# Kernel tuning notes

Measured on AMD Instinct MI355X. Metric: run time of the kernel, lower is better.

## Reference

```python
import jax, jax.numpy as jnp
import numpy as np

TEMP = 0.05


def _l2norm(x, axis=-1, eps=1e-12):
    n = jnp.sqrt(jnp.sum(x * x, axis=axis, keepdims=True))
    return x / jnp.maximum(n, eps)


def setup_inputs() -> dict:
    key = jax.random.key(0)
    k1, k2, k3 = jax.random.split(key, 3)
    B, D, N = 1024, 2048, 16384
    inputs = jax.random.normal(k1, (B, D), dtype=jnp.float32)
    targets = jax.random.randint(k2, (B,), 0, N, dtype=jnp.int32).astype(jnp.int64)
    # cluster memory bank: initialized to unit-norm centroids (buffer is zeros in
    # torch but is always filled with normalized centroids before use)
    features = _l2norm(jax.random.normal(k3, (N, D), dtype=jnp.float32))
    return {"inputs": inputs, "targets": targets, "features": features}


def reference(inputs, targets, features):
    # ClusterMemory.forward: normalize -> cosine sim vs bank -> / temp
    xn = _l2norm(inputs, axis=1)            # [B, D]
    out = (xn @ features.T) / TEMP          # [B, N]
    return out
```

## Files before the change

### kernel.cpp

```cpp
#include <hip/hip_runtime.h>
#include <hip/hip_bf16.h>


typedef short  bf16x8 __attribute__((ext_vector_type(8)));
typedef float  f32x4  __attribute__((ext_vector_type(4)));
typedef float  f32x16 __attribute__((ext_vector_type(16)));

#define D_K   2048
#define N_N   16384
#define M_M   1024
#define TEMP_INV 20.0f

__device__ __forceinline__ unsigned short f2bf(float f) {
    unsigned u = __builtin_bit_cast(unsigned, f);
    u += 0x7FFFu + ((u >> 16) & 1u);
    return (unsigned short)(u >> 16);
}

#define GLOAD16(g, l) __builtin_amdgcn_global_load_lds(                        \
    (const __attribute__((address_space(1))) unsigned int*)(g),                \
    (__attribute__((address_space(3))) unsigned int*)(l), 16, 0, 0)

__global__ __launch_bounds__(256) void prep_kernel(const float* __restrict__ x,
                                                   const float* __restrict__ B,
                                                   unsigned short* __restrict__ abf,
                                                   unsigned short* __restrict__ bbf) {
    int t = threadIdx.x;
    if (blockIdx.x < M_M) {
        int row = blockIdx.x;
        const float4* xr = reinterpret_cast<const float4*>(x + (size_t)row * D_K);
        float4 a = xr[t * 2];
        float4 b = xr[t * 2 + 1];
        float s = a.x*a.x + a.y*a.y + a.z*a.z + a.w*a.w
                + b.x*b.x + b.y*b.y + b.z*b.z + b.w*b.w;
        #pragma unroll
        for (int off = 32; off > 0; off >>= 1) s += __shfl_down(s, off);
        __shared__ float ps[4];
        __shared__ float sbc;
        if ((t & 63) == 0) ps[t >> 6] = s;
        __syncthreads();
        if (t == 0) {
            float tot = ps[0] + ps[1] + ps[2] + ps[3];
            sbc = 1.0f / fmaxf(sqrtf(tot), 1e-12f);
        }
        __syncthreads();
        float rs = sbc;
        bf16x8 v;
        v[0] = (short)f2bf(a.x * rs); v[1] = (short)f2bf(a.y * rs);
        v[2] = (short)f2bf(a.z * rs); v[3] = (short)f2bf(a.w * rs);
        v[4] = (short)f2bf(b.x * rs); v[5] = (short)f2bf(b.y * rs);
        v[6] = (short)f2bf(b.z * rs); v[7] = (short)f2bf(b.w * rs);
        *reinterpret_cast<bf16x8*>(abf + (size_t)row * D_K + t * 8) = v;
    } else {
        const size_t nv = (size_t)N_N * D_K / 8;
        size_t stride = (size_t)(gridDim.x - M_M) * blockDim.x;
        for (size_t v = (size_t)(blockIdx.x - M_M) * blockDim.x + t; v < nv; v += stride) {
            const float4* p = reinterpret_cast<const float4*>(B) + v * 2;
            float4 a = p[0], b = p[1];
            bf16x8 o;
            o[0] = (short)f2bf(a.x); o[1] = (short)f2bf(a.y);
            o[2] = (short)f2bf(a.z); o[3] = (short)f2bf(a.w);
            o[4] = (short)f2bf(b.x); o[5] = (short)f2bf(b.y);
            o[6] = (short)f2bf(b.z); o[7] = (short)f2bf(b.w);
            reinterpret_cast<bf16x8*>(bbf)[v] = o;
        }
    }
}

__global__ __launch_bounds__(512, 2) void gemm32_kernel(const unsigned short* __restrict__ Abf,
                                                        const unsigned short* __restrict__ Bbf,
                                                        float* __restrict__ C) {
    __shared__ __align__(16) unsigned short lds[65536];

    int bid = blockIdx.x;
    int wg  = (bid & 7) * 32 + (bid >> 3);
    int tm  = wg & 3, tn = wg >> 2;
    int m_blk = tm * 256, n_blk = tn * 256;

    int t = threadIdx.x, lane = t & 63, w = t >> 6;
    int wm = w >> 2, wn = w & 3;

    int row31 = lane & 31, khalf = lane >> 5;
    int xorm  = (row31 >> 1) & 3;
    int slotk[2], aao[4], bbo[2];
    #pragma unroll
    for (int kk = 0; kk < 2; ++kk) slotk[kk] = ((kk * 2 + khalf) ^ xorm) * 16;
    #pragma unroll
    for (int rb = 0; rb < 4; ++rb) aao[rb] = (wm * 128 + rb * 32 + row31) * 64;
    #pragma unroll
    for (int cb = 0; cb < 2; ++cb) bbo[cb] = (wn * 64 + cb * 32 + row31) * 64;

    const unsigned short* gA[2];
    const unsigned short* gB[2];
    int sdst[2];
    #pragma unroll
    for (int pass = 0; pass < 2; ++pass) {
        int r = pass * 128 + (t >> 2);
        int csrc = (t & 3) ^ ((r >> 1) & 3);
        gA[pass] = Abf + (size_t)(m_blk + r) * D_K + csrc * 8;
        gB[pass] = Bbf + (size_t)(n_blk + r) * D_K + csrc * 8;
        sdst[pass] = pass * 8192 + w * 1024;
    }

    auto stage = [&](int mat, int s, int b, int ktile) {
        int kt = ktile < 32 ? ktile : 31;
        int koff = kt * 64 + s * 32;
        int ldsb = b * 65536 + mat * 32768 + s * 16384;
        GLOAD16((mat ? gB[0] : gA[0]) + koff, (char*)lds + ldsb + sdst[0]);
        GLOAD16((mat ? gB[1] : gA[1]) + koff, (char*)lds + ldsb + sdst[1]);
    };

    f32x16 acc[4][2] = {};

#define PHASE32(bb, ss, ST1, ST2)                                              \
    {                                                                          \
        char* abase = (char*)lds + (bb) * 65536 + (ss) * 16384;                \
        char* bbase = abase + 32768;                                           \
        bf16x8 af[4][2], bv[2][2];                                             \
        _Pragma("unroll")                                                      \
        for (int rb = 0; rb < 4; ++rb)                                         \
            _Pragma("unroll")                                                  \
            for (int kk = 0; kk < 2; ++kk)                                     \
                af[rb][kk] = *reinterpret_cast<const bf16x8*>(                 \
                    abase + aao[rb] + slotk[kk]);                              \
        _Pragma("unroll")                                                      \
        for (int cb = 0; cb < 2; ++cb)                                         \
            _Pragma("unroll")                                                  \
            for (int kk = 0; kk < 2; ++kk)                                     \
                bv[cb][kk] = *reinterpret_cast<const bf16x8*>(                 \
                    bbase + bbo[cb] + slotk[kk]);                              \
        ST1;                                                                   \
        ST2;                                                                   \
        asm volatile("s_barrier" ::: "memory");                                \
        asm volatile("s_waitcnt lgkmcnt(0)" ::: "memory");                     \
        __builtin_amdgcn_sched_barrier(0);                                     \
        __builtin_amdgcn_s_setprio(1);                                         \
        _Pragma("unroll")                                                      \
        for (int kk = 0; kk < 2; ++kk)                                         \
            _Pragma("unroll")                                                  \
            for (int rb = 0; rb < 4; ++rb)                                     \
                _Pragma("unroll")                                              \
                for (int cb = 0; cb < 2; ++cb)                                 \
                    acc[rb][cb] = __builtin_amdgcn_mfma_f32_32x32x16_bf16(     \
                        af[rb][kk], bv[cb][kk], acc[rb][cb], 0, 0, 0);         \
        __builtin_amdgcn_s_setprio(0);                                         \
        asm volatile("s_waitcnt vmcnt(8)" ::: "memory");                       \
        asm volatile("s_barrier" ::: "memory");                                \
    }

    stage(0, 0, 0, 0);
    stage(1, 0, 0, 0);
    stage(0, 1, 0, 0);
    stage(1, 1, 0, 0);
    stage(0, 0, 1, 1);
    stage(1, 0, 1, 1);
    asm volatile("s_waitcnt vmcnt(8)" ::: "memory");
    asm volatile("s_barrier" ::: "memory");

    for (int T = 0; T < 32; ++T) {
        int b = T & 1;
        PHASE32(b, 0, stage(0, 1, b ^ 1, T + 1), stage(1, 1, b ^ 1, T + 1))
        PHASE32(b, 1, stage(0, 0, b,     T + 2), stage(1, 0, b,     T + 2))
    }
#undef PHASE32

    #pragma unroll
    for (int rb = 0; rb < 4; ++rb)
        #pragma unroll
        for (int cb = 0; cb < 2; ++cb) {
            int colg = n_blk + wn * 64 + cb * 32 + row31;
            #pragma unroll
            for (int r = 0; r < 16; ++r) {
                int rowg = m_blk + wm * 128 + rb * 32 +
                           (r & 3) + 8 * (r >> 2) + 4 * khalf;
                C[(size_t)rowg * N_N + colg] = acc[rb][cb][r] * TEMP_INV;
            }
        }
}

__global__ __launch_bounds__(256) void rnorm_kernel(const float* __restrict__ x,
                                                    float* __restrict__ rn) {
    int row = blockIdx.x;
    const float4* xr = reinterpret_cast<const float4*>(x + (size_t)row * D_K);
    int t = threadIdx.x;
    float4 a = xr[t];
    float4 b = xr[t + 256];
    float s = a.x*a.x + a.y*a.y + a.z*a.z + a.w*a.w
            + b.x*b.x + b.y*b.y + b.z*b.z + b.w*b.w;
    #pragma unroll
    for (int off = 32; off > 0; off >>= 1) s += __shfl_down(s, off);
    __shared__ float ps[4];
    int wave = t >> 6, lane = t & 63;
    if (lane == 0) ps[wave] = s;
    __syncthreads();
    if (t == 0) {
        float tot = ps[0] + ps[1] + ps[2] + ps[3];
        rn[row] = 1.0f / fmaxf(sqrtf(tot), 1e-12f);
    }
}

__global__ __launch_bounds__(256, 2) void gemm_kernel(const float* __restrict__ A,
                                                      const float* __restrict__ Bm,
                                                      const float* __restrict__ rn,
                                                      float* __restrict__ C) {
    constexpr int BK = 64;
    __shared__ __align__(16) short lAs[128 * BK];
    __shared__ __align__(16) short lBs[128 * BK];
    int bid = blockIdx.x;
    int nb  = (bid & 7) * 128 + (bid >> 3);
    int tm  = nb & 7;
    int tn  = nb >> 3;
    int m0 = tm * 128, n0 = tn * 128;
    int t = threadIdx.x;
    int lane = t & 63, w = t >> 6;
    int wr = (w >> 1) * 64, wc = (w & 1) * 64;
    f32x4 acc[4][4] = {};
    float4 ra[4][2], rb[4][2];
    float  sc[4];
    int    srow[4], sgrp[4];
    #pragma unroll
    for (int i = 0; i < 4; ++i) {
        int li = t + i * 256;
        srow[i] = li >> 3;
        sgrp[i] = li & 7;
        sc[i]   = rn[m0 + srow[i]];
    }
    auto load_tiles = [&](int kt) {
        int k0 = kt * BK;
        #pragma unroll
        for (int i = 0; i < 4; ++i) {
            const float4* pa = reinterpret_cast<const float4*>(
                A + (size_t)(m0 + srow[i]) * D_K + k0 + sgrp[i] * 8);
            ra[i][0] = pa[0]; ra[i][1] = pa[1];
            const float4* pb = reinterpret_cast<const float4*>(
                Bm + (size_t)(n0 + srow[i]) * D_K + k0 + sgrp[i] * 8);
            rb[i][0] = pb[0]; rb[i][1] = pb[1];
        }
    };
    auto write_tiles = [&]() {
        #pragma unroll
        for (int i = 0; i < 4; ++i) {
            int row = srow[i];
            int slotw = sgrp[i] ^ (row & 7);
            float s = sc[i];
            bf16x8 va, vb;
            va[0] = (short)f2bf(ra[i][0].x * s); va[1] = (short)f2bf(ra[i][0].y * s);
            va[2] = (short)f2bf(ra[i][0].z * s); va[3] = (short)f2bf(ra[i][0].w * s);
            va[4] = (short)f2bf(ra[i][1].x * s); va[5] = (short)f2bf(ra[i][1].y * s);
            va[6] = (short)f2bf(ra[i][1].z * s); va[7] = (short)f2bf(ra[i][1].w * s);
            vb[0] = (short)f2bf(rb[i][0].x); vb[1] = (short)f2bf(rb[i][0].y);
            vb[2] = (short)f2bf(rb[i][0].z); vb[3] = (short)f2bf(rb[i][0].w);
            vb[4] = (short)f2bf(rb[i][1].x); vb[5] = (short)f2bf(rb[i][1].y);
            vb[6] = (short)f2bf(rb[i][1].z); vb[7] = (short)f2bf(rb[i][1].w);
            *reinterpret_cast<bf16x8*>(&lAs[row * BK + slotw * 8]) = va;
            *reinterpret_cast<bf16x8*>(&lBs[row * BK + slotw * 8]) = vb;
        }
    };
    auto compute = [&]() {
        #pragma unroll
        for (int ks = 0; ks < 2; ++ks) {
            bf16x8 af[4], bfr[4];
            #pragma unroll
            for (int f = 0; f < 4; ++f) {
                int arow = wr + f * 16 + (lane & 15);
                int aslot = (ks * 4 + (lane >> 4)) ^ (arow & 7);
                af[f] = *reinterpret_cast<const bf16x8*>(&lAs[arow * BK + aslot * 8]);
                int brow = wc + f * 16 + (lane & 15);
                int bslot = (ks * 4 + (lane >> 4)) ^ (brow & 7);
                bfr[f] = *reinterpret_cast<const bf16x8*>(&lBs[brow * BK + bslot * 8]);
            }
            #pragma unroll
            for (int m = 0; m < 4; ++m)
                #pragma unroll
                for (int n = 0; n < 4; ++n)
                    acc[m][n] = __builtin_amdgcn_mfma_f32_16x16x32_bf16(
                        af[m], bfr[n], acc[m][n], 0, 0, 0);
        }
    };
    load_tiles(0);
    write_tiles();
    for (int kt = 1; kt < D_K / BK; ++kt) {
        __syncthreads();
        load_tiles(kt);
        compute();
        __syncthreads();
        write_tiles();
    }
    __syncthreads();
    compute();
    #pragma unroll
    for (int m = 0; m < 4; ++m) {
        int r = m0 + wr + m * 16 + (lane >> 4) * 4;
        #pragma unroll
        for (int j = 0; j < 4; ++j) {
            float* cp = C + (size_t)(r + j) * N_N + n0 + wc + (lane & 15);
            #pragma unroll
            for (int n = 0; n < 4; ++n)
                cp[n * 16] = acc[m][n][j] * TEMP_INV;
        }
    }
}

extern "C" void kernel_launch(void* const* d_in, const int* in_sizes, int n_in,
                              void* d_out, int out_size, void* d_ws, size_t ws_size,
                              hipStream_t stream) {
    const float* inputs   = (const float*)d_in[0];
    const float* features = (const float*)d_in[2];
    float* out = (float*)d_out;

    const size_t needA = (size_t)M_M * D_K * 2;
    const size_t needB = (size_t)N_N * D_K * 2;
    if (ws_size >= needA + needB) {
        unsigned short* Abf = (unsigned short*)d_ws;
        unsigned short* Bbf = Abf + (size_t)M_M * D_K;
        prep_kernel<<<M_M + 2048, 256, 0, stream>>>(inputs, features, Abf, Bbf);
        gemm32_kernel<<<(M_M / 256) * (N_N / 256), 512, 0, stream>>>(Abf, Bbf, out);
    } else {
        float* rn = (float*)d_ws;
        rnorm_kernel<<<M_M, 256, 0, stream>>>(inputs, rn);
        gemm_kernel<<<(M_M / 128) * (N_N / 128), 256, 0, stream>>>(inputs, features, rn, out);
    }
}
```

Measured before the change: 113.2 us.

## Switch GEMM to 128x512 tiles with 16x16x32 MFMA and single-block occupancy

Replaces the 256x256-tile GEMM, which used 32x32x16 MFMAs and two blocks per CU, with a 128x512 tile that uses 16x16x32 MFMAs, one block per CU and 160 KB of double-buffered LDS. Each wave now computes a 64x128 sub-tile, and every global-to-LDS stage loads one A slice plus four B slices. The intent is to cut A re-reads per output, get more B reuse per A load, and produce more contiguous row-major output stores. In exchange, occupancy drops to one block per CU and the MFMA shape changes, which can hurt latency hiding.

```diff
diff --git a/kernel.cpp b/kernel.cpp
--- a/kernel.cpp
+++ b/kernel.cpp
@@ -2,9 +2,8 @@
 #include <hip/hip_bf16.h>
 
 
-typedef short  bf16x8 __attribute__((ext_vector_type(8)));
-typedef float  f32x4  __attribute__((ext_vector_type(4)));
-typedef float  f32x16 __attribute__((ext_vector_type(16)));
+typedef short bf16x8 __attribute__((ext_vector_type(8)));
+typedef float f32x4  __attribute__((ext_vector_type(4)));
 
 #define D_K   2048
 #define N_N   16384
@@ -67,115 +66,105 @@
     }
 }
 
-__global__ __launch_bounds__(512, 2) void gemm32_kernel(const unsigned short* __restrict__ Abf,
-                                                        const unsigned short* __restrict__ Bbf,
-                                                        float* __restrict__ C) {
-    __shared__ __align__(16) unsigned short lds[65536];
+__global__ __launch_bounds__(512, 1) void gemmw_kernel(const unsigned short* __restrict__ Abf,
+                                                       const unsigned short* __restrict__ Bbf,
+                                                       float* __restrict__ C) {
+    __shared__ __align__(16) unsigned short lds[81920];
 
     int bid = blockIdx.x;
     int wg  = (bid & 7) * 32 + (bid >> 3);
-    int tm  = wg & 3, tn = wg >> 2;
-    int m_blk = tm * 256, n_blk = tn * 256;
+    int tm  = wg & 7, tn = wg >> 3;
+    int m_blk = tm * 128, n_blk = tn * 512;
 
     int t = threadIdx.x, lane = t & 63, w = t >> 6;
     int wm = w >> 2, wn = w & 3;
 
-    int row31 = lane & 31, khalf = lane >> 5;
-    int xorm  = (row31 >> 1) & 3;
-    int slotk[2], aao[4], bbo[2];
-    #pragma unroll
-    for (int kk = 0; kk < 2; ++kk) slotk[kk] = ((kk * 2 + khalf) ^ xorm) * 16;
-    #pragma unroll
-    for (int rb = 0; rb < 4; ++rb) aao[rb] = (wm * 128 + rb * 32 + row31) * 64;
-    #pragma unroll
-    for (int cb = 0; cb < 2; ++cb) bbo[cb] = (wn * 64 + cb * 32 + row31) * 64;
-
-    const unsigned short* gA[2];
-    const unsigned short* gB[2];
-    int sdst[2];
-    #pragma unroll
-    for (int pass = 0; pass < 2; ++pass) {
-        int r = pass * 128 + (t >> 2);
-        int csrc = (t & 3) ^ ((r >> 1) & 3);
-        gA[pass] = Abf + (size_t)(m_blk + r) * D_K + csrc * 8;
-        gB[pass] = Bbf + (size_t)(n_blk + r) * D_K + csrc * 8;
-        sdst[pass] = pass * 8192 + w * 1024;
-    }
-
-    auto stage = [&](int mat, int s, int b, int ktile) {
+    int l15  = lane & 15;
+    int slot = ((lane >> 4) ^ ((l15 >> 1) & 3)) * 16;
+    int aoff[4], boff[8];
+    #pragma unroll
+    for (int rb = 0; rb < 4; ++rb)
+        aoff[rb] = (wm * 64 + rb * 16 + l15) * 64 + slot;
+    #pragma unroll
+    for (int cb = 0; cb < 8; ++cb)
+        boff[cb] = (wn * 128 + cb * 16 + l15) * 64 + slot;
+
+    int rA = t >> 2;
+    int cA = (t & 3) ^ ((rA >> 1) & 3);
+    const unsigned short* gA0 = Abf + (size_t)(m_blk + rA) * D_K + cA * 8;
+    const unsigned short* gB[4];
+    #pragma unroll
+    for (int p = 0; p < 4; ++p) {
+        int r = p * 128 + (t >> 2);
+        int c = (t & 3) ^ ((r >> 1) & 3);
+        gB[p] = Bbf + (size_t)(n_blk + r) * D_K + c * 8;
+    }
+    int sdst = w * 1024;
+
+    auto stageS = [&](int s, int b, int ktile) {
         int kt = ktile < 32 ? ktile : 31;
         int koff = kt * 64 + s * 32;
-        int ldsb = b * 65536 + mat * 32768 + s * 16384;
-        GLOAD16((mat ? gB[0] : gA[0]) + koff, (char*)lds + ldsb + sdst[0]);
-        GLOAD16((mat ? gB[1] : gA[1]) + koff, (char*)lds + ldsb + sdst[1]);
+        char* dst = (char*)lds + b * 81920;
+        GLOAD16(gA0 + koff, dst + s * 8192 + sdst);
+        #pragma unroll
+        for (int p = 0; p < 4; ++p)
+            GLOAD16(gB[p] + koff, dst + 16384 + s * 32768 + p * 8192 + sdst);
     };
 
-    f32x16 acc[4][2] = {};
-
-#define PHASE32(bb, ss, ST1, ST2)                                              \
+    f32x4 acc[4][8] = {};
+
+#define PHASEW(b, s, STS, STB, STKT)                                           \
     {                                                                          \
-        char* abase = (char*)lds + (bb) * 65536 + (ss) * 16384;                \
-        char* bbase = abase + 32768;                                           \
-        bf16x8 af[4][2], bv[2][2];                                             \
+        char* base = (char*)lds + (b) * 81920;                                 \
+        bf16x8 af[4], bv[8];                                                   \
         _Pragma("unroll")                                                      \
         for (int rb = 0; rb < 4; ++rb)                                         \
-            _Pragma("unroll")                                                  \
-            for (int kk = 0; kk < 2; ++kk)                                     \
-                af[rb][kk] = *reinterpret_cast<const bf16x8*>(                 \
-                    abase + aao[rb] + slotk[kk]);                              \
+            af[rb] = *reinterpret_cast<const bf16x8*>(                         \
+                base + (s) * 8192 + aoff[rb]);                                 \
         _Pragma("unroll")                                                      \
-        for (int cb = 0; cb < 2; ++cb)                                         \
-            _Pragma("unroll")                                                  \
-            for (int kk = 0; kk < 2; ++kk)                                     \
-                bv[cb][kk] = *reinterpret_cast<const bf16x8*>(                 \
-                    bbase + bbo[cb] + slotk[kk]);                              \
-        ST1;                                                                   \
-        ST2;                                                                   \
+        for (int cb = 0; cb < 8; ++cb)                                         \
+            bv[cb] = *reinterpret_cast<const bf16x8*>(                         \
+                base + 16384 + (s) * 32768 + boff[cb]);                        \
+        stageS(STS, STB, STKT);                                                \
         asm volatile("s_barrier" ::: "memory");                                \
         asm volatile("s_waitcnt lgkmcnt(0)" ::: "memory");                     \
         __builtin_amdgcn_sched_barrier(0);                                     \
         __builtin_amdgcn_s_setprio(1);                                         \
         _Pragma("unroll")                                                      \
-        for (int kk = 0; kk < 2; ++kk)                                         \
+        for (int cb = 0; cb < 8; ++cb)                                         \
             _Pragma("unroll")                                                  \
             for (int rb = 0; rb < 4; ++rb)                                     \
-                _Pragma("unroll")                                              \
-                for (int cb = 0; cb < 2; ++cb)                                 \
-                    acc[rb][cb] = __builtin_amdgcn_mfma_f32_32x32x16_bf16(     \
-                        af[rb][kk], bv[cb][kk], acc[rb][cb], 0, 0, 0);         \
+                acc[rb][cb] = __builtin_amdgcn_mfma_f32_16x16x32_bf16(         \
+                    af[rb], bv[cb], acc[rb][cb], 0, 0, 0);                     \
         __builtin_amdgcn_s_setprio(0);                                         \
-        asm volatile("s_waitcnt vmcnt(8)" ::: "memory");                       \
+        asm volatile("s_waitcnt vmcnt(10)" ::: "memory");                      \
         asm volatile("s_barrier" ::: "memory");                                \
     }
 
-    stage(0, 0, 0, 0);
-    stage(1, 0, 0, 0);
-    stage(0, 1, 0, 0);
-    stage(1, 1, 0, 0);
-    stage(0, 0, 1, 1);
-    stage(1, 0, 1, 1);
-    asm volatile("s_waitcnt vmcnt(8)" ::: "memory");
+    stageS(0, 0, 0);
+    stageS(1, 0, 0);
+    stageS(0, 1, 1);
+    asm volatile("s_waitcnt vmcnt(10)" ::: "memory");
     asm volatile("s_barrier" ::: "memory");
 
     for (int T = 0; T < 32; ++T) {
         int b = T & 1;
-        PHASE32(b, 0, stage(0, 1, b ^ 1, T + 1), stage(1, 1, b ^ 1, T + 1))
-        PHASE32(b, 1, stage(0, 0, b,     T + 2), stage(1, 0, b,     T + 2))
-    }
-#undef PHASE32
-
-    #pragma unroll
-    for (int rb = 0; rb < 4; ++rb)
-        #pragma unroll
-        for (int cb = 0; cb < 2; ++cb) {
-            int colg = n_blk + wn * 64 + cb * 32 + row31;
+        PHASEW(b, 0, 1, b ^ 1, T + 1)
+        PHASEW(b, 1, 0, b,     T + 2)
+    }
+#undef PHASEW
+
+    #pragma unroll
+    for (int rb = 0; rb < 4; ++rb) {
+        int r = m_blk + wm * 64 + rb * 16 + (lane >> 4) * 4;
+        #pragma unroll
+        for (int j = 0; j < 4; ++j) {
+            float* cp = C + (size_t)(r + j) * N_N + n_blk + wn * 128 + (lane & 15);
             #pragma unroll
-            for (int r = 0; r < 16; ++r) {
-                int rowg = m_blk + wm * 128 + rb * 32 +
-                           (r & 3) + 8 * (r >> 2) + 4 * khalf;
-                C[(size_t)rowg * N_N + colg] = acc[rb][cb][r] * TEMP_INV;
-            }
-        }
+            for (int cb = 0; cb < 8; ++cb)
+                cp[cb * 16] = acc[rb][cb][j] * TEMP_INV;
+        }
+    }
 }
 
 __global__ __launch_bounds__(256) void rnorm_kernel(const float* __restrict__ x,
@@ -314,7 +303,7 @@
         unsigned short* Abf = (unsigned short*)d_ws;
         unsigned short* Bbf = Abf + (size_t)M_M * D_K;
         prep_kernel<<<M_M + 2048, 256, 0, stream>>>(inputs, features, Abf, Bbf);
-        gemm32_kernel<<<(M_M / 256) * (N_N / 256), 512, 0, stream>>>(Abf, Bbf, out);
+        gemmw_kernel<<<(M_M / 128) * (N_N / 512), 512, 0, stream>>>(Abf, Bbf, out);
     } else {
         float* rn = (float*)d_ws;
         rnorm_kernel<<<M_M, 256, 0, stream>>>(inputs, rn);
```

After: 109.6 us. 3.1% less time.
